# Kernel tuning notes

Measured on AMD Instinct MI355X. Metric: run time of the kernel, lower is better.

The kernel has to match this reference:

```python
import jax, jax.numpy as jnp
import numpy as np

D = 512        # d_model
H = 8          # num_heads
DH = D // H    # d_head
HID = 2048     # ffn hidden
L = 6          # num_layers
S = 512        # src len
T = 512        # tgt len
VS = 16000     # src vocab
VT = 16000     # tgt vocab
B = 4
PAD = 0
EPS = 1e-5
SCALE = 0.02


def setup_inputs() -> dict:
    key = jax.random.key(0)
    ks = jax.random.split(key, 24)
    # tokens in [1, V), then force trailing pads
    src = jax.random.randint(ks[0], (B, S), 1, VS, dtype=jnp.int32).at[:, -32:].set(PAD)
    tgt = jax.random.randint(ks[1], (B, T), 1, VT, dtype=jnp.int32).at[:, -32:].set(PAD)
    n = lambda k, shp: (jax.random.normal(k, shp, dtype=jnp.float32) * SCALE)
    return {
        "src": src, "tgt": tgt,
        "emb_src": n(ks[2], (VS, D)),
        "emb_tgt": n(ks[3], (VT, D)),
        "enc_attn_w": n(ks[4], (L, 4, D, D)),
        "enc_attn_b": n(ks[5], (L, 4, D)),
        "enc_ff_w1": n(ks[6], (L, D, HID)),
        "enc_ff_b1": n(ks[7], (L, HID)),
        "enc_ff_w2": n(ks[8], (L, HID, D)),
        "enc_ff_b2": n(ks[9], (L, D)),
        "enc_ln_g": jnp.ones((L, 2, D), jnp.float32),
        "enc_ln_b": jnp.zeros((L, 2, D), jnp.float32),
        "dec_attn_w": n(ks[10], (L, 2, 4, D, D)),  # [:,0]=self, [:,1]=cross
        "dec_attn_b": n(ks[11], (L, 2, 4, D)),
        "dec_ff_w1": n(ks[12], (L, D, HID)),
        "dec_ff_b1": n(ks[13], (L, HID)),
        "dec_ff_w2": n(ks[14], (L, HID, D)),
        "dec_ff_b2": n(ks[15], (L, D)),
        "dec_ln_g": jnp.ones((L, 3, D), jnp.float32),
        "dec_ln_b": jnp.zeros((L, 3, D), jnp.float32),
        "fc_w": n(ks[16], (D, VT)),
        "fc_b": jnp.zeros((VT,), jnp.float32),
    }


def _pos_encoding(seq_len, d):
    pos = jnp.arange(seq_len, dtype=jnp.float32)[:, None]
    div = jnp.exp(jnp.arange(0, d, 2, dtype=jnp.float32) * (-np.log(10000.0) / d))
    pe = jnp.zeros((seq_len, d), jnp.float32)
    pe = pe.at[:, 0::2].set(jnp.sin(pos * div))
    pe = pe.at[:, 1::2].set(jnp.cos(pos * div))
    return pe


def _layer_norm(x, g, b):
    m = jnp.mean(x, axis=-1, keepdims=True)
    v = jnp.mean((x - m) ** 2, axis=-1, keepdims=True)
    return (x - m) / jnp.sqrt(v + EPS) * g + b


def _mha(xq, xkv, w, b, mask):
    # w: [4, D, D] (q,k,v,o), b: [4, D]; mask True = masked
    def proj(x, wi, bi):
        y = x @ wi + bi
        return y.reshape(y.shape[0], y.shape[1], H, DH).transpose(0, 2, 1, 3)  # [B,H,S,dh]
    Q, K, V = proj(xq, w[0], b[0]), proj(xkv, w[1], b[1]), proj(xkv, w[2], b[2])
    scores = jnp.einsum('bhqd,bhkd->bhqk', Q, K) / jnp.sqrt(jnp.float32(DH))
    if mask is not None:
        scores = jnp.where(mask, -jnp.inf, scores)
    attn = jax.nn.softmax(scores, axis=-1)
    out = jnp.einsum('bhqk,bhkd->bhqd', attn, V).transpose(0, 2, 1, 3).reshape(xq.shape[0], xq.shape[1], D)
    return out @ w[3] + b[3]


def reference(src, tgt, emb_src, emb_tgt,
              enc_attn_w, enc_attn_b, enc_ff_w1, enc_ff_b1, enc_ff_w2, enc_ff_b2,
              enc_ln_g, enc_ln_b,
              dec_attn_w, dec_attn_b, dec_ff_w1, dec_ff_b1, dec_ff_w2, dec_ff_b2,
              dec_ln_g, dec_ln_b, fc_w, fc_b):
    pe = _pos_encoding(max(S, T), D)
    enc = emb_src[src] + pe[:S]
    dec = emb_tgt[tgt] + pe[:T]
    src_mask = (src == PAD)[:, None, None, :]                        # [B,1,1,S]
    causal = jnp.triu(jnp.ones((T, T), bool), k=1)                   # [T,T]
    tgt_mask = causal[None, None] | (tgt == PAD)[:, None, None, :]   # [B,1,T,T]
    for l in range(L):
        a = _mha(enc, enc, enc_attn_w[l], enc_attn_b[l], src_mask)
        enc = _layer_norm(enc + a, enc_ln_g[l, 0], enc_ln_b[l, 0])
        f = jax.nn.relu(enc @ enc_ff_w1[l] + enc_ff_b1[l]) @ enc_ff_w2[l] + enc_ff_b2[l]
        enc = _layer_norm(enc + f, enc_ln_g[l, 1], enc_ln_b[l, 1])
    for l in range(L):
        a = _mha(dec, dec, dec_attn_w[l, 0], dec_attn_b[l, 0], tgt_mask)
        dec = _layer_norm(dec + a, dec_ln_g[l, 0], dec_ln_b[l, 0])
        a = _mha(dec, enc, dec_attn_w[l, 1], dec_attn_b[l, 1], src_mask)
        dec = _layer_norm(dec + a, dec_ln_g[l, 1], dec_ln_b[l, 1])
        f = jax.nn.relu(dec @ dec_ff_w1[l] + dec_ff_b1[l]) @ dec_ff_w2[l] + dec_ff_b2[l]
        dec = _layer_norm(dec + f, dec_ln_g[l, 2], dec_ln_b[l, 2])
    return dec @ fc_w + fc_b  # [B,T,VT]
```

## Files before the change

kernel.cpp:

```cpp
#include <hip/hip_runtime.h>
#include <math.h>

#define D 512
#define NH 8
#define DH 64
#define HID 2048
#define NL 6
#define SEQ 512
#define BATCH 4
#define MROWS (BATCH * SEQ)
#define NVT 16000
#define LNEPS 1e-5f

typedef __attribute__((ext_vector_type(8))) short short8;
typedef __attribute__((ext_vector_type(4))) float f32x4;

__device__ __forceinline__ ushort bf16_rtne(float f) {
    uint u = __builtin_bit_cast(uint, f);
    return (ushort)((u + 0x7fffu + ((u >> 16) & 1u)) >> 16);
}
__device__ __forceinline__ uint rtne2(float a, float b) {
    return (uint)bf16_rtne(a) | ((uint)bf16_rtne(b) << 16);
}

__global__ __launch_bounds__(256) void wsplit_kernel(const float* __restrict__ src,
                                                     ushort* __restrict__ dst,
                                                     int K, int N, size_t zstride) {
    __shared__ float T[64][65];
    src += (size_t)blockIdx.z * zstride;
    dst += (size_t)blockIdx.z * zstride;
    const int t = threadIdx.x;
    const int n0 = blockIdx.x * 64;
    const int k0 = blockIdx.y * 64;
    {
        const int kr = t >> 4, nc = (t & 15) * 4;
#pragma unroll
        for (int i = 0; i < 4; ++i) {
            float4 v = *(const float4*)&src[(size_t)(k0 + kr + 16 * i) * N + n0 + nc];
            T[kr + 16 * i][nc + 0] = v.x;
            T[kr + 16 * i][nc + 1] = v.y;
            T[kr + 16 * i][nc + 2] = v.z;
            T[kr + 16 * i][nc + 3] = v.w;
        }
    }
    __syncthreads();
    const int n = t >> 2;
    const int kc = (t & 3) * 16;
    uint h[8];
#pragma unroll
    for (int i = 0; i < 8; ++i)
        h[i] = rtne2(T[kc + 2 * i][n], T[kc + 2 * i + 1][n]);
    ushort* dh = &dst[(size_t)(n0 + n) * K + k0 + kc];
    *(uint4*)(dh + 0) = uint4{h[0], h[1], h[2], h[3]};
    *(uint4*)(dh + 8) = uint4{h[4], h[5], h[6], h[7]};
}

template <int BM, int BN, bool RELU>
__global__ __launch_bounds__(256) void gemm_mfma(const float* __restrict__ A0,
                                                 const float* __restrict__ A1,
                                                 const ushort* __restrict__ WT,
                                                 const float* __restrict__ bias,
                                                 float* __restrict__ C,
                                                 int M, int N, int K,
                                                 size_t wz, size_t cz) {
    constexpr int FM = BM / 32;
    constexpr int FN = BN / 32;
    constexpr int EA = BM / 32;
    constexpr int EB = BN / 64;
    constexpr int AROW = 40;

    __shared__ ushort Ah[BM * AROW];
    __shared__ ushort Bh[BN * AROW];

    const float* A = (blockIdx.z == 0) ? A0 : A1;
    WT += (size_t)blockIdx.z * wz;
    bias += (size_t)blockIdx.z * (size_t)N;
    C += (size_t)blockIdx.z * cz;

    const int tid = threadIdx.x;
    const int lane = tid & 63;
    const int wv = tid >> 6;
    const int wm = wv >> 1, wn = wv & 1;
    const int bm = blockIdx.x * BM;
    const int bn = blockIdx.y * BN;

    const int a_m = tid >> 3;
    const int a_kk = (tid & 7) * 4;
    const int b_n = tid >> 2;
    const int b_kq = (tid & 3) * 8;

    const float* aP[EA];
#pragma unroll
    for (int i = 0; i < EA; ++i)
        aP[i] = A + (size_t)(bm + 32 * i + a_m) * K + a_kk;
    const ushort* bP[EB];
#pragma unroll
    for (int i = 0; i < EB; ++i)
        bP[i] = WT + (size_t)(bn + 64 * i + b_n) * K + b_kq;

    f32x4 apre[EA];
    uint4 bpre[EB];
#pragma unroll
    for (int i = 0; i < EA; ++i) apre[i] = *(const f32x4*)(aP[i]);
#pragma unroll
    for (int i = 0; i < EB; ++i) bpre[i] = *(const uint4*)(bP[i]);

    f32x4 acc[FM][FN] = {};

    const int NT = K >> 5;
    for (int kt = 0; kt < NT; ++kt) {
#pragma unroll
        for (int i = 0; i < EA; ++i) {
            const int idx = (32 * i + a_m) * AROW + a_kk;
            *(uint2*)&Ah[idx] = uint2{rtne2(apre[i][0], apre[i][1]),
                                      rtne2(apre[i][2], apre[i][3])};
        }
#pragma unroll
        for (int i = 0; i < EB; ++i)
            *(uint4*)&Bh[(64 * i + b_n) * AROW + b_kq] = bpre[i];
        __syncthreads();

        if (kt + 1 < NT) {
            const int ko = (kt + 1) * 32;
#pragma unroll
            for (int i = 0; i < EA; ++i) apre[i] = *(const f32x4*)(aP[i] + ko);
#pragma unroll
            for (int i = 0; i < EB; ++i) bpre[i] = *(const uint4*)(bP[i] + ko);
        }

        const int g8 = (lane >> 4) * 8;
        short8 af[FM], bf[FN];
#pragma unroll
        for (int mi = 0; mi < FM; ++mi)
            af[mi] = *(const short8*)&Ah[(wm * (BM / 2) + mi * 16 + (lane & 15)) * AROW + g8];
#pragma unroll
        for (int ni = 0; ni < FN; ++ni)
            bf[ni] = *(const short8*)&Bh[(wn * (BN / 2) + ni * 16 + (lane & 15)) * AROW + g8];

#pragma unroll
        for (int ni = 0; ni < FN; ++ni)
#pragma unroll
            for (int mi = 0; mi < FM; ++mi)
                acc[mi][ni] = __builtin_amdgcn_mfma_f32_16x16x32_bf16(af[mi], bf[ni], acc[mi][ni], 0, 0, 0);
        __syncthreads();
    }

#pragma unroll
    for (int ni = 0; ni < FN; ++ni) {
        const int col = bn + wn * (BN / 2) + ni * 16 + (lane & 15);
        const float bv = bias[col];
#pragma unroll
        for (int mi = 0; mi < FM; ++mi) {
            const int r0 = bm + wm * (BM / 2) + mi * 16 + (lane >> 4) * 4;
#pragma unroll
            for (int r = 0; r < 4; ++r) {
                float v = acc[mi][ni][r] + bv;
                if (RELU) v = fmaxf(v, 0.0f);
                C[(size_t)(r0 + r) * N + col] = v;
            }
        }
    }
}

template <int MODE>
__global__ __launch_bounds__(256) void attn_mfma(const float* __restrict__ Qm,
                                                 const float* __restrict__ Km,
                                                 const float* __restrict__ Vm,
                                                 const int* __restrict__ toks,
                                                 float* __restrict__ Om) {
    constexpr int ROW = 72;
    __shared__ ushort Kl[64 * ROW];
    __shared__ ushort Vl[64 * ROW];
    __shared__ ushort Pl[4][16 * ROW];

    const int tid = threadIdx.x;
    const int lane = tid & 63;
    const int w = tid >> 6;
    const int g = lane >> 4, c = lane & 15;
    const int b = blockIdx.y >> 3, h = blockIdx.y & 7;
    const int q0 = blockIdx.x * 64;
    const size_t base = (size_t)b * SEQ * D + h * DH;
    const int* tokp = toks + b * SEQ;

    short8 qf[2];
    {
        const float* qp = Qm + base + (size_t)(q0 + w * 16 + c) * D + g * 8;
#pragma unroll
        for (int kc = 0; kc < 2; ++kc) {
            union { ushort us[8]; short8 s8; } u;
#pragma unroll
            for (int i = 0; i < 8; ++i) u.us[i] = bf16_rtne(qp[kc * 32 + i]);
            qf[kc] = u.s8;
        }
    }

    const int sk_key = tid >> 2, sk_dh = (tid & 3) * 16;
    const int sv_dh = tid >> 2, sv_key = (tid & 3) * 16;
    const float* kP = Km + base + (size_t)sk_key * D + sk_dh;
    const float* vP = Vm + base + (size_t)sv_key * D + sv_dh;

    f32x4 kreg[4];
    float vreg[16];
#pragma unroll
    for (int j = 0; j < 4; ++j) kreg[j] = *(const f32x4*)(kP + 4 * j);
#pragma unroll
    for (int i = 0; i < 16; ++i) vreg[i] = vP[(size_t)i * D];

    f32x4 Ov[4] = {};
    float m_r[4], l_r[4];
#pragma unroll
    for (int r = 0; r < 4; ++r) { m_r[r] = -1e30f; l_r[r] = 0.f; }

    for (int kt = 0; kt < SEQ / 64; ++kt) {
        {
            union { ushort us[16]; uint4 u4[2]; } uk, uv;
#pragma unroll
            for (int j = 0; j < 4; ++j)
#pragma unroll
                for (int i = 0; i < 4; ++i) uk.us[4 * j + i] = bf16_rtne(kreg[j][i]);
#pragma unroll
            for (int i = 0; i < 16; ++i) uv.us[i] = bf16_rtne(vreg[i]);
            *(uint4*)&Kl[sk_key * ROW + sk_dh + 0] = uk.u4[0];
            *(uint4*)&Kl[sk_key * ROW + sk_dh + 8] = uk.u4[1];
            *(uint4*)&Vl[sv_dh * ROW + sv_key + 0] = uv.u4[0];
            *(uint4*)&Vl[sv_dh * ROW + sv_key + 8] = uv.u4[1];
        }
        __syncthreads();

        if (kt + 1 < SEQ / 64) {
            const size_t adv = (size_t)(kt + 1) * 64 * D;
#pragma unroll
            for (int j = 0; j < 4; ++j) kreg[j] = *(const f32x4*)(kP + adv + 4 * j);
#pragma unroll
            for (int i = 0; i < 16; ++i) vreg[i] = vP[adv + (size_t)i * D];
        }

        f32x4 sc[4] = {};
#pragma unroll
        for (int ni = 0; ni < 4; ++ni)
#pragma unroll
            for (int kc = 0; kc < 2; ++kc) {
                short8 kf = *(const short8*)&Kl[(ni * 16 + c) * ROW + kc * 32 + g * 8];
                sc[ni] = __builtin_amdgcn_mfma_f32_16x16x32_bf16(qf[kc], kf, sc[ni], 0, 0, 0);
            }

        const int k0g = kt * 64;
        int tk[4];
#pragma unroll
        for (int ni = 0; ni < 4; ++ni) tk[ni] = tokp[k0g + ni * 16 + c];
        float p[4][4], tm[4];
#pragma unroll
        for (int r = 0; r < 4; ++r) tm[r] = -1e30f;
#pragma unroll
        for (int ni = 0; ni < 4; ++ni) {
            const int key = k0g + ni * 16 + c;
            const bool colmask = (tk[ni] == 0);
#pragma unroll
            for (int r = 0; r < 4; ++r) {
                bool msk = colmask;
                if (MODE == 1) msk = msk || (key > q0 + w * 16 + 4 * g + r);
                const float s = msk ? -1e30f : sc[ni][r] * 0.125f;
                p[ni][r] = s;
                tm[r] = fmaxf(tm[r], s);
            }
        }
#pragma unroll
        for (int off = 1; off < 16; off <<= 1)
#pragma unroll
            for (int r = 0; r < 4; ++r) tm[r] = fmaxf(tm[r], __shfl_xor(tm[r], off, 16));
        float f_r[4], ts[4];
#pragma unroll
        for (int r = 0; r < 4; ++r) {
            const float mn = fmaxf(m_r[r], tm[r]);
            f_r[r] = __expf(m_r[r] - mn);
            m_r[r] = mn;
            ts[r] = 0.f;
        }
#pragma unroll
        for (int ni = 0; ni < 4; ++ni)
#pragma unroll
            for (int r = 0; r < 4; ++r) {
                const float e = (p[ni][r] <= -1e29f) ? 0.f : __expf(p[ni][r] - m_r[r]);
                p[ni][r] = e;
                ts[r] += e;
            }
#pragma unroll
        for (int off = 1; off < 16; off <<= 1)
#pragma unroll
            for (int r = 0; r < 4; ++r) ts[r] += __shfl_xor(ts[r], off, 16);
#pragma unroll
        for (int r = 0; r < 4; ++r) l_r[r] = l_r[r] * f_r[r] + ts[r];
#pragma unroll
        for (int nd = 0; nd < 4; ++nd)
#pragma unroll
            for (int r = 0; r < 4; ++r) Ov[nd][r] *= f_r[r];

#pragma unroll
        for (int ni = 0; ni < 4; ++ni)
#pragma unroll
            for (int r = 0; r < 4; ++r)
                Pl[w][(4 * r + g) * ROW + ni * 16 + c] = bf16_rtne(p[ni][r]);
        asm volatile("s_waitcnt lgkmcnt(0)" ::: "memory");
        __builtin_amdgcn_sched_barrier(0);

        const int pr = ((c & 3) << 2) | (c >> 2);
#pragma unroll
        for (int kc = 0; kc < 2; ++kc) {
            short8 pf = *(const short8*)&Pl[w][pr * ROW + kc * 32 + g * 8];
#pragma unroll
            for (int nd = 0; nd < 4; ++nd) {
                short8 vf = *(const short8*)&Vl[(nd * 16 + c) * ROW + kc * 32 + g * 8];
                Ov[nd] = __builtin_amdgcn_mfma_f32_16x16x32_bf16(pf, vf, Ov[nd], 0, 0, 0);
            }
        }
        __syncthreads();
    }

    float inv[4];
#pragma unroll
    for (int r = 0; r < 4; ++r) inv[r] = 1.0f / l_r[r];
    float* op = Om + base;
#pragma unroll
    for (int nd = 0; nd < 4; ++nd)
#pragma unroll
        for (int r = 0; r < 4; ++r)
            op[(size_t)(q0 + w * 16 + 4 * g + r) * D + nd * 16 + c] = Ov[nd][r] * inv[r];
}

__global__ __launch_bounds__(128) void embed_kernel(const int* __restrict__ toks,
                                                    const float* __restrict__ emb,
                                                    float* __restrict__ out) {
    const int row = blockIdx.x;
    const int s = row & (SEQ - 1);
    const int tok = toks[row];
    const int d = threadIdx.x * 4;
    float4 e = *(const float4*)&emb[tok * D + d];
    float r[4];
#pragma unroll
    for (int i = 0; i < 4; i += 2) {
        const int dd = d + i;
        const float dv = expf((float)dd * (-9.210340371976184f / (float)D));
        const float ang = (float)s * dv;
        r[i] = sinf(ang);
        r[i + 1] = cosf(ang);
    }
    float4 o;
    o.x = e.x + r[0]; o.y = e.y + r[1]; o.z = e.z + r[2]; o.w = e.w + r[3];
    *(float4*)&out[row * D + d] = o;
}

__global__ __launch_bounds__(128) void add_ln_kernel(float* __restrict__ x,
                                                     const float* __restrict__ r,
                                                     const float* __restrict__ g,
                                                     const float* __restrict__ b) {
    const int row = blockIdx.x;
    const int t = threadIdx.x;
    const int d = t * 4;
    float4 xv = *(const float4*)&x[row * D + d];
    float4 rv = *(const float4*)&r[row * D + d];
    float4 v;
    v.x = xv.x + rv.x; v.y = xv.y + rv.y; v.z = xv.z + rv.z; v.w = xv.w + rv.w;
    float s = v.x + v.y + v.z + v.w;
    float s2 = v.x * v.x + v.y * v.y + v.z * v.z + v.w * v.w;
#pragma unroll
    for (int off = 32; off > 0; off >>= 1) {
        s += __shfl_down(s, off);
        s2 += __shfl_down(s2, off);
    }
    __shared__ float sh[4];
    if ((t & 63) == 0) { sh[(t >> 6) * 2] = s; sh[(t >> 6) * 2 + 1] = s2; }
    __syncthreads();
    s = sh[0] + sh[2];
    s2 = sh[1] + sh[3];
    const float mean = s * (1.0f / D);
    const float var = s2 * (1.0f / D) - mean * mean;
    const float rstd = rsqrtf(var + LNEPS);
    float4 gv = *(const float4*)&g[d];
    float4 bv = *(const float4*)&b[d];
    float4 o;
    o.x = (v.x - mean) * rstd * gv.x + bv.x;
    o.y = (v.y - mean) * rstd * gv.y + bv.y;
    o.z = (v.z - mean) * rstd * gv.z + bv.z;
    o.w = (v.w - mean) * rstd * gv.w + bv.w;
    *(float4*)&x[row * D + d] = o;
}

extern "C" void kernel_launch(void* const* d_in, const int* in_sizes, int n_in,
                              void* d_out, int out_size, void* d_ws, size_t ws_size,
                              hipStream_t stream) {
    const int* src = (const int*)d_in[0];
    const int* tgt = (const int*)d_in[1];
    const float* emb_src = (const float*)d_in[2];
    const float* emb_tgt = (const float*)d_in[3];
    const float* enc_attn_w = (const float*)d_in[4];
    const float* enc_attn_b = (const float*)d_in[5];
    const float* enc_ff_w1 = (const float*)d_in[6];
    const float* enc_ff_b1 = (const float*)d_in[7];
    const float* enc_ff_w2 = (const float*)d_in[8];
    const float* enc_ff_b2 = (const float*)d_in[9];
    const float* enc_ln_g = (const float*)d_in[10];
    const float* enc_ln_b = (const float*)d_in[11];
    const float* dec_attn_w = (const float*)d_in[12];
    const float* dec_attn_b = (const float*)d_in[13];
    const float* dec_ff_w1 = (const float*)d_in[14];
    const float* dec_ff_b1 = (const float*)d_in[15];
    const float* dec_ff_w2 = (const float*)d_in[16];
    const float* dec_ff_b2 = (const float*)d_in[17];
    const float* dec_ln_g = (const float*)d_in[18];
    const float* dec_ln_b = (const float*)d_in[19];
    const float* fc_w = (const float*)d_in[20];
    const float* fc_b = (const float*)d_in[21];
    float* out = (float*)d_out;

    float* ws = (float*)d_ws;
    const size_t NTOK = (size_t)MROWS * D;
    float* xe = ws;
    float* xd = xe + NTOK;
    float* qb = xd + NTOK;
    float* kb = qb + NTOK;
    float* vb = kb + NTOK;
    float* ab = vb + NTOK;
    float* tb = ab + NTOK;
    float* hb = tb + NTOK;
    ushort* u0 = (ushort*)(hb + (size_t)MROWS * HID);
    const size_t DD = (size_t)D * D;
    ushort* wA = u0;
    ushort* wF1 = wA + 8 * DD;
    ushort* wF2 = wF1 + DD * 4;
    ushort* wFC = wF2 + DD * 4;

    auto transpose = [&](const float* w, ushort* dh, int K, int N, int nz) {
        dim3 grid(N / 64, K / 64, nz);
        wsplit_kernel<<<grid, 256, 0, stream>>>(w, dh, K, N, (size_t)K * N);
    };
    auto gemm64 = [&](const float* A, const ushort* WT,
                      const float* bias, float* C, int M, int N, int K) {
        dim3 grid(M / 64, N / 64, 1);
        gemm_mfma<64, 64, false><<<grid, 256, 0, stream>>>(A, A, WT, bias, C, M, N, K, 0, 0);
    };
    auto gemm128 = [&](const float* A, const ushort* WT,
                       const float* bias, float* C, int M, int N, int K, bool relu) {
        dim3 grid(M / 128, N / 128, 1);
        if (relu)
            gemm_mfma<128, 128, true><<<grid, 256, 0, stream>>>(A, A, WT, bias, C, M, N, K, 0, 0);
        else
            gemm_mfma<128, 128, false><<<grid, 256, 0, stream>>>(A, A, WT, bias, C, M, N, K, 0, 0);
    };
    auto gemm_qkv = [&](const float* Aq, const float* Akv,
                        const ushort* WT, const float* bi) {
        dim3 grid(MROWS / 128, D / 128, 3);
        gemm_mfma<128, 128, false><<<grid, 256, 0, stream>>>(Aq, Akv, WT, bi, qb,
                                                             MROWS, D, D, DD, NTOK);
    };

    embed_kernel<<<MROWS, 128, 0, stream>>>(src, emb_src, xe);
    embed_kernel<<<MROWS, 128, 0, stream>>>(tgt, emb_tgt, xd);

    const dim3 attn_grid(SEQ / 64, BATCH * NH);

    for (int l = 0; l < NL; ++l) {
        const float* bi = enc_attn_b + (size_t)l * 4 * D;
        transpose(enc_attn_w + (size_t)l * 4 * DD, wA, D, D, 4);
        transpose(enc_ff_w1 + (size_t)l * D * HID, wF1, D, HID, 1);
        transpose(enc_ff_w2 + (size_t)l * HID * D, wF2, HID, D, 1);

        gemm_qkv(xe, xe, wA, bi);
        attn_mfma<0><<<attn_grid, 256, 0, stream>>>(qb, kb, vb, src, ab);
        gemm64(ab, wA + 3 * DD, bi + 3 * D, tb, MROWS, D, D);
        add_ln_kernel<<<MROWS, 128, 0, stream>>>(xe, tb,
            enc_ln_g + (size_t)(l * 2 + 0) * D, enc_ln_b + (size_t)(l * 2 + 0) * D);
        gemm128(xe, wF1, enc_ff_b1 + (size_t)l * HID, hb, MROWS, HID, D, true);
        gemm64(hb, wF2, enc_ff_b2 + (size_t)l * D, tb, MROWS, D, HID);
        add_ln_kernel<<<MROWS, 128, 0, stream>>>(xe, tb,
            enc_ln_g + (size_t)(l * 2 + 1) * D, enc_ln_b + (size_t)(l * 2 + 1) * D);
    }

    for (int l = 0; l < NL; ++l) {
        transpose(dec_attn_w + (size_t)l * 8 * DD, wA, D, D, 8);
        transpose(dec_ff_w1 + (size_t)l * D * HID, wF1, D, HID, 1);
        transpose(dec_ff_w2 + (size_t)l * HID * D, wF2, HID, D, 1);
        {
            const float* bi = dec_attn_b + (size_t)(l * 2 + 0) * 4 * D;
            gemm_qkv(xd, xd, wA, bi);
            attn_mfma<1><<<attn_grid, 256, 0, stream>>>(qb, kb, vb, tgt, ab);
            gemm64(ab, wA + 3 * DD, bi + 3 * D, tb, MROWS, D, D);
            add_ln_kernel<<<MROWS, 128, 0, stream>>>(xd, tb,
                dec_ln_g + (size_t)(l * 3 + 0) * D, dec_ln_b + (size_t)(l * 3 + 0) * D);
        }
        {
            const float* bi = dec_attn_b + (size_t)(l * 2 + 1) * 4 * D;
            gemm_qkv(xd, xe, wA + 4 * DD, bi);
            attn_mfma<0><<<attn_grid, 256, 0, stream>>>(qb, kb, vb, src, ab);
            gemm64(ab, wA + 7 * DD, bi + 3 * D, tb, MROWS, D, D);
            add_ln_kernel<<<MROWS, 128, 0, stream>>>(xd, tb,
                dec_ln_g + (size_t)(l * 3 + 1) * D, dec_ln_b + (size_t)(l * 3 + 1) * D);
        }
        gemm128(xd, wF1, dec_ff_b1 + (size_t)l * HID, hb, MROWS, HID, D, true);
        gemm64(hb, wF2, dec_ff_b2 + (size_t)l * D, tb, MROWS, D, HID);
        add_ln_kernel<<<MROWS, 128, 0, stream>>>(xd, tb,
            dec_ln_g + (size_t)(l * 3 + 2) * D, dec_ln_b + (size_t)(l * 3 + 2) * D);
    }

    transpose(fc_w, wFC, D, NVT, 1);
    {
        dim3 grid(MROWS / 128, NVT / 128, 1);
        gemm_mfma<128, 128, false><<<grid, 256, 0, stream>>>(xd, xd, wFC, fc_b, out,
                                                             MROWS, NVT, D, 0, 0);
    }
}
```

Baseline: 2.336 ms.

## Double-buffer GEMM LDS tiles, batch weight conversion, retile QKV, fuse embeddings

The GEMM kernel now double-buffers its LDS tiles so the next k-slice is written while the current one feeds MFMA, leaving one barrier per iteration instead of two. When the workspace is large enough, all layer weights are converted to bf16 up front in a few large launches instead of three small launches per layer. The QKV projection switches from 128x128 to 64x64 tiles to get more blocks, and the two embedding launches are merged into one. The cost is twice the LDS per block, which may lower occupancy, plus a larger workspace requirement; the per-layer conversion path is kept as a fallback.

```diff
diff --git a/kernel.cpp b/kernel.cpp
--- a/kernel.cpp
+++ b/kernel.cpp
@@ -69,8 +69,8 @@
     constexpr int EB = BN / 64;
     constexpr int AROW = 40;
 
-    __shared__ ushort Ah[BM * AROW];
-    __shared__ ushort Bh[BN * AROW];
+    __shared__ ushort Ah[2][BM * AROW];
+    __shared__ ushort Bh[2][BN * AROW];
 
     const float* A = (blockIdx.z == 0) ? A0 : A1;
     WT += (size_t)blockIdx.z * wz;
@@ -106,42 +106,59 @@
     for (int i = 0; i < EB; ++i) bpre[i] = *(const uint4*)(bP[i]);
 
     f32x4 acc[FM][FN] = {};
-
     const int NT = K >> 5;
-    for (int kt = 0; kt < NT; ++kt) {
-#pragma unroll
-        for (int i = 0; i < EA; ++i) {
-            const int idx = (32 * i + a_m) * AROW + a_kk;
-            *(uint2*)&Ah[idx] = uint2{rtne2(apre[i][0], apre[i][1]),
-                                      rtne2(apre[i][2], apre[i][3])};
-        }
-#pragma unroll
-        for (int i = 0; i < EB; ++i)
-            *(uint4*)&Bh[(64 * i + b_n) * AROW + b_kq] = bpre[i];
-        __syncthreads();
-
-        if (kt + 1 < NT) {
-            const int ko = (kt + 1) * 32;
-#pragma unroll
-            for (int i = 0; i < EA; ++i) apre[i] = *(const f32x4*)(aP[i] + ko);
-#pragma unroll
-            for (int i = 0; i < EB; ++i) bpre[i] = *(const uint4*)(bP[i] + ko);
-        }
-
-        const int g8 = (lane >> 4) * 8;
+
+#pragma unroll
+    for (int i = 0; i < EA; ++i) {
+        const int idx = (32 * i + a_m) * AROW + a_kk;
+        *(uint2*)&Ah[0][idx] = uint2{rtne2(apre[i][0], apre[i][1]),
+                                     rtne2(apre[i][2], apre[i][3])};
+    }
+#pragma unroll
+    for (int i = 0; i < EB; ++i)
+        *(uint4*)&Bh[0][(64 * i + b_n) * AROW + b_kq] = bpre[i];
+    if (NT > 1) {
+#pragma unroll
+        for (int i = 0; i < EA; ++i) apre[i] = *(const f32x4*)(aP[i] + 32);
+#pragma unroll
+        for (int i = 0; i < EB; ++i) bpre[i] = *(const uint4*)(bP[i] + 32);
+    }
+    __syncthreads();
+
+    const int g8 = (lane >> 4) * 8;
+    for (int t = 0; t < NT; ++t) {
+        const int cur = t & 1;
         short8 af[FM], bf[FN];
 #pragma unroll
         for (int mi = 0; mi < FM; ++mi)
-            af[mi] = *(const short8*)&Ah[(wm * (BM / 2) + mi * 16 + (lane & 15)) * AROW + g8];
+            af[mi] = *(const short8*)&Ah[cur][(wm * (BM / 2) + mi * 16 + (lane & 15)) * AROW + g8];
 #pragma unroll
         for (int ni = 0; ni < FN; ++ni)
-            bf[ni] = *(const short8*)&Bh[(wn * (BN / 2) + ni * 16 + (lane & 15)) * AROW + g8];
-
+            bf[ni] = *(const short8*)&Bh[cur][(wn * (BN / 2) + ni * 16 + (lane & 15)) * AROW + g8];
 #pragma unroll
         for (int ni = 0; ni < FN; ++ni)
 #pragma unroll
             for (int mi = 0; mi < FM; ++mi)
                 acc[mi][ni] = __builtin_amdgcn_mfma_f32_16x16x32_bf16(af[mi], bf[ni], acc[mi][ni], 0, 0, 0);
+
+        if (t + 1 < NT) {
+#pragma unroll
+            for (int i = 0; i < EA; ++i) {
+                const int idx = (32 * i + a_m) * AROW + a_kk;
+                *(uint2*)&Ah[cur ^ 1][idx] = uint2{rtne2(apre[i][0], apre[i][1]),
+                                                   rtne2(apre[i][2], apre[i][3])};
+            }
+#pragma unroll
+            for (int i = 0; i < EB; ++i)
+                *(uint4*)&Bh[cur ^ 1][(64 * i + b_n) * AROW + b_kq] = bpre[i];
+            if (t + 2 < NT) {
+                const int ko = (t + 2) * 32;
+#pragma unroll
+                for (int i = 0; i < EA; ++i) apre[i] = *(const f32x4*)(aP[i] + ko);
+#pragma unroll
+                for (int i = 0; i < EB; ++i) bpre[i] = *(const uint4*)(bP[i] + ko);
+            }
+        }
         __syncthreads();
     }
 
@@ -327,9 +344,16 @@
             op[(size_t)(q0 + w * 16 + 4 * g + r) * D + nd * 16 + c] = Ov[nd][r] * inv[r];
 }
 
-__global__ __launch_bounds__(128) void embed_kernel(const int* __restrict__ toks,
-                                                    const float* __restrict__ emb,
-                                                    float* __restrict__ out) {
+__global__ __launch_bounds__(128) void embed2_kernel(const int* __restrict__ src,
+                                                     const int* __restrict__ tgt,
+                                                     const float* __restrict__ es,
+                                                     const float* __restrict__ et,
+                                                     float* __restrict__ xe,
+                                                     float* __restrict__ xd) {
+    const int which = blockIdx.y;
+    const int* toks = which ? tgt : src;
+    const float* emb = which ? et : es;
+    float* out = which ? xd : xe;
     const int row = blockIdx.x;
     const int s = row & (SEQ - 1);
     const int tok = toks[row];
@@ -424,12 +448,29 @@
     float* hb = tb + NTOK;
     ushort* u0 = (ushort*)(hb + (size_t)MROWS * HID);
     const size_t DD = (size_t)D * D;
-    ushort* wA = u0;
-    ushort* wF1 = wA + 8 * DD;
-    ushort* wF2 = wF1 + DD * 4;
-    ushort* wFC = wF2 + DD * 4;
-
-    auto transpose = [&](const float* w, ushort* dh, int K, int N, int nz) {
+    const size_t FCE = (size_t)D * NVT;
+    const size_t act_bytes = (size_t)(7 * NTOK + (size_t)MROWS * HID) * 4;
+    const bool batched = ws_size >= act_bytes + (168 * DD + FCE) * 2 + 1024;
+
+    ushort *bEncA, *bEncF1, *bEncF2, *bDecA, *bDecF1, *bDecF2, *bFC;
+    ushort *wA = nullptr, *wF1 = nullptr, *wF2 = nullptr;
+    if (batched) {
+        bEncA = u0;
+        bEncF1 = bEncA + 24 * DD;
+        bEncF2 = bEncF1 + 24 * DD;
+        bDecA = bEncF2 + 24 * DD;
+        bDecF1 = bDecA + 48 * DD;
+        bDecF2 = bDecF1 + 24 * DD;
+        bFC = bDecF2 + 24 * DD;
+    } else {
+        wA = u0;
+        wF1 = wA + 8 * DD;
+        wF2 = wF1 + 4 * DD;
+        bFC = wF2 + 4 * DD;
+        bEncA = bEncF1 = bEncF2 = bDecA = bDecF1 = bDecF2 = nullptr;
+    }
+
+    auto tr = [&](const float* w, ushort* dh, int K, int N, int nz) {
         dim3 grid(N / 64, K / 64, nz);
         wsplit_kernel<<<grid, 256, 0, stream>>>(w, dh, K, N, (size_t)K * N);
     };
@@ -448,63 +489,92 @@
     };
     auto gemm_qkv = [&](const float* Aq, const float* Akv,
                         const ushort* WT, const float* bi) {
-        dim3 grid(MROWS / 128, D / 128, 3);
-        gemm_mfma<128, 128, false><<<grid, 256, 0, stream>>>(Aq, Akv, WT, bi, qb,
-                                                             MROWS, D, D, DD, NTOK);
+        dim3 grid(MROWS / 64, D / 64, 3);
+        gemm_mfma<64, 64, false><<<grid, 256, 0, stream>>>(Aq, Akv, WT, bi, qb,
+                                                           MROWS, D, D, DD, NTOK);
     };
 
-    embed_kernel<<<MROWS, 128, 0, stream>>>(src, emb_src, xe);
-    embed_kernel<<<MROWS, 128, 0, stream>>>(tgt, emb_tgt, xd);
+    if (batched) {
+        tr(enc_attn_w, bEncA, D, D, 4 * NL);
+        tr(enc_ff_w1, bEncF1, D, HID, NL);
+        tr(enc_ff_w2, bEncF2, HID, D, NL);
+        tr(dec_attn_w, bDecA, D, D, 8 * NL);
+        tr(dec_ff_w1, bDecF1, D, HID, NL);
+        tr(dec_ff_w2, bDecF2, HID, D, NL);
+        tr(fc_w, bFC, D, NVT, 1);
+    }
+
+    embed2_kernel<<<dim3(MROWS, 2), 128, 0, stream>>>(src, tgt, emb_src, emb_tgt, xe, xd);
 
     const dim3 attn_grid(SEQ / 64, BATCH * NH);
 
     for (int l = 0; l < NL; ++l) {
         const float* bi = enc_attn_b + (size_t)l * 4 * D;
-        transpose(enc_attn_w + (size_t)l * 4 * DD, wA, D, D, 4);
-        transpose(enc_ff_w1 + (size_t)l * D * HID, wF1, D, HID, 1);
-        transpose(enc_ff_w2 + (size_t)l * HID * D, wF2, HID, D, 1);
-
-        gemm_qkv(xe, xe, wA, bi);
+        ushort* eA;
+        ushort* eF1;
+        ushort* eF2;
+        if (batched) {
+            eA = bEncA + (size_t)l * 4 * DD;
+            eF1 = bEncF1 + (size_t)l * 4 * DD;
+            eF2 = bEncF2 + (size_t)l * 4 * DD;
+        } else {
+            eA = wA; eF1 = wF1; eF2 = wF2;
+            tr(enc_attn_w + (size_t)l * 4 * DD, wA, D, D, 4);
+            tr(enc_ff_w1 + (size_t)l * D * HID, wF1, D, HID, 1);
+            tr(enc_ff_w2 + (size_t)l * HID * D, wF2, HID, D, 1);
+        }
+
+        gemm_qkv(xe, xe, eA, bi);
         attn_mfma<0><<<attn_grid, 256, 0, stream>>>(qb, kb, vb, src, ab);
-        gemm64(ab, wA + 3 * DD, bi + 3 * D, tb, MROWS, D, D);
+        gemm64(ab, eA + 3 * DD, bi + 3 * D, tb, MROWS, D, D);
         add_ln_kernel<<<MROWS, 128, 0, stream>>>(xe, tb,
             enc_ln_g + (size_t)(l * 2 + 0) * D, enc_ln_b + (size_t)(l * 2 + 0) * D);
-        gemm128(xe, wF1, enc_ff_b1 + (size_t)l * HID, hb, MROWS, HID, D, true);
-        gemm64(hb, wF2, enc_ff_b2 + (size_t)l * D, tb, MROWS, D, HID);
+        gemm128(xe, eF1, enc_ff_b1 + (size_t)l * HID, hb, MROWS, HID, D, true);
+        gemm64(hb, eF2, enc_ff_b2 + (size_t)l * D, tb, MROWS, D, HID);
         add_ln_kernel<<<MROWS, 128, 0, stream>>>(xe, tb,
             enc_ln_g + (size_t)(l * 2 + 1) * D, enc_ln_b + (size_t)(l * 2 + 1) * D);
     }
 
     for (int l = 0; l < NL; ++l) {
-        transpose(dec_attn_w + (size_t)l * 8 * DD, wA, D, D, 8);
-        transpose(dec_ff_w1 + (size_t)l * D * HID, wF1, D, HID, 1);
-        transpose(dec_ff_w2 + (size_t)l * HID * D, wF2, HID, D, 1);
+        ushort* dA;
+        ushort* dF1;
+        ushort* dF2;
+        if (batched) {
+            dA = bDecA + (size_t)l * 8 * DD;
+            dF1 = bDecF1 + (size_t)l * 4 * DD;
+            dF2 = bDecF2 + (size_t)l * 4 * DD;
+        } else {
+            dA = wA; dF1 = wF1; dF2 = wF2;
+            tr(dec_attn_w + (size_t)l * 8 * DD, wA, D, D, 8);
+            tr(dec_ff_w1 + (size_t)l * D * HID, wF1, D, HID, 1);
+            tr(dec_ff_w2 + (size_t)l * HID * D, wF2, HID, D, 1);
+        }
         {
             const float* bi = dec_attn_b + (size_t)(l * 2 + 0) * 4 * D;
-            gemm_qkv(xd, xd, wA, bi);
+            gemm_qkv(xd, xd, dA, bi);
             attn_mfma<1><<<attn_grid, 256, 0, stream>>>(qb, kb, vb, tgt, ab);
-            gemm64(ab, wA + 3 * DD, bi + 3 * D, tb, MROWS, D, D);
+            gemm64(ab, dA + 3 * DD, bi + 3 * D, tb, MROWS, D, D);
             add_ln_kernel<<<MROWS, 128, 0, stream>>>(xd, tb,
                 dec_ln_g + (size_t)(l * 3 + 0) * D, dec_ln_b + (size_t)(l * 3 + 0) * D);
         }
         {
             const float* bi = dec_attn_b + (size_t)(l * 2 + 1) * 4 * D;
-            gemm_qkv(xd, xe, wA + 4 * DD, bi);
+            gemm_qkv(xd, xe, dA + 4 * DD, bi);
             attn_mfma<0><<<attn_grid, 256, 0, stream>>>(qb, kb, vb, src, ab);
-            gemm64(ab, wA + 7 * DD, bi + 3 * D, tb, MROWS, D, D);
+            gemm64(ab, dA + 7 * DD, bi + 3 * D, tb, MROWS, D, D);
             add_ln_kernel<<<MROWS, 128, 0, stream>>>(xd, tb,
                 dec_ln_g + (size_t)(l * 3 + 1) * D, dec_ln_b + (size_t)(l * 3 + 1) * D);
         }
-        gemm128(xd, wF1, dec_ff_b1 + (size_t)l * HID, hb, MROWS, HID, D, true);
-        gemm64(hb, wF2, dec_ff_b2 + (size_t)l * D, tb, MROWS, D, HID);
+        gemm128(xd, dF1, dec_ff_b1 + (size_t)l * HID, hb, MROWS, HID, D, true);
+        gemm64(hb, dF2, dec_ff_b2 + (size_t)l * D, tb, MROWS, D, HID);
         add_ln_kernel<<<MROWS, 128, 0, stream>>>(xd, tb,
             dec_ln_g + (size_t)(l * 3 + 2) * D, dec_ln_b + (size_t)(l * 3 + 2) * D);
     }
 
-    transpose(fc_w, wFC, D, NVT, 1);
+    if (!batched) tr(fc_w, bFC, D, NVT, 1);
     {
         dim3 grid(MROWS / 128, NVT / 128, 1);
-        gemm_mfma<128, 128, false><<<grid, 256, 0, stream>>>(xd, xd, wFC, fc_b, out,
+        gemm_mfma<128, 128, false><<<grid, 256, 0, stream>>>(xd, xd, bFC, fc_b, out,
                                                              MROWS, NVT, D, 0, 0);
     }
 }
```

Result: faster. 2.039 ms (-12.7%).
